# Optimization experiments

Hardware: AMD Instinct MI355X
Metric: run time of the kernel (lower is better)

Reference implementation:

```python
import jax, jax.numpy as jnp
import numpy as np


def setup_inputs() -> dict:
    key = jax.random.key(0)
    ks = jax.random.split(key, 6)
    B, Nab, Nag, d, K = 16, 16384, 16384, 128, 10
    return {
        "H1": jax.random.normal(ks[0], (B, Nab, d), jnp.float32),
        "H2": jax.random.normal(ks[1], (B, Nag, d), jnp.float32),
        "X1": jax.random.normal(ks[2], (B, Nab, 3), jnp.float32),
        "X2": jax.random.normal(ks[3], (B, Nag, 3), jnp.float32),
        "W1": jax.random.uniform(ks[4], (K, d, d), jnp.float32),
        "W2": jax.random.uniform(ks[5], (K, d, d), jnp.float32),
    }


def _kabsch(P, Q):
    # Rigid alignment: find R (3x3), t (3,) s.t. P @ R + t ~= Q (least squares).
    c1 = P.mean(axis=0)
    c2 = Q.mean(axis=0)
    Pc = P - c1
    Qc = Q - c2
    Hm = Pc.T @ Qc  # [3,3] covariance
    U, S, Vt = jnp.linalg.svd(Hm, full_matrices=False)
    sign = jnp.sign(jnp.linalg.det(U @ Vt))
    Dm = jnp.diag(jnp.concatenate([jnp.ones(2, dtype=P.dtype), sign[None]]))
    R = U @ Dm @ Vt
    t = c2 - c1 @ R
    return P @ R + t, R, t


def reference(H1, H2, X1, X2, W1, W2):
    # Keypoint cross-attention. Faithful to torch:
    #   alpha_1k = softmax( (H1 @ W1_k @ H2.T).mean(dim=1) / sqrt(d) )
    # Using mean-over-columns identity: (H1 @ W @ H2.T).mean(1) = H1 @ W @ mean(H2,0)
    d = H1.shape[-1]
    scale = 1.0 / np.sqrt(d)
    h2bar = H2.mean(axis=1)  # [B, d]
    h1bar = H1.mean(axis=1)  # [B, d]
    v1 = jnp.einsum('kde,be->bkd', W1, h2bar)          # W1_k @ mean(H2)
    s1 = jnp.einsum('bnd,bkd->bkn', H1, v1) * scale     # [B, K, Nab]
    a1 = jax.nn.softmax(s1, axis=-1)
    Y1 = jnp.einsum('bkn,bnc->bkc', a1, X1)             # [B, K, 3]
    v2 = jnp.einsum('kde,be->bkd', W2, h1bar)
    s2 = jnp.einsum('bmd,bkd->bkm', H2, v2) * scale     # [B, K, Nag]
    a2 = jax.nn.softmax(s2, axis=-1)
    Y2 = jnp.einsum('bkm,bmc->bkc', a2, X2)             # [B, K, 3]
    Y1_aligned, R, t = jax.vmap(_kabsch)(Y1, Y2)
    return jnp.stack([Y1, Y2, Y1_aligned], axis=1)      # [B, 3, K, 3]
```

## Files before the change

### kernel.cpp

```cpp
#include <hip/hip_runtime.h>
#include <math.h>

#define NB 16
#define NN 16384
#define DD 128
#define KK 10

#define WS_FLOATS 46336


__global__ __launch_bounds__(256) void k_mean2(const float* __restrict__ H2,
                                               float* __restrict__ hsum) {
    int tid = threadIdx.x, b = blockIdx.x;
    int batch = b >> 7, sub = b & 127;
    int c0 = tid & 15;
    int rofs = sub * 16 + (tid >> 4);
    const float4* H4 = (const float4*)H2 + (size_t)batch * (NN * (DD / 4));

    float4 a0 = make_float4(0.f, 0.f, 0.f, 0.f), a1 = a0;
    float4 h0 = H4[(size_t)rofs * 32 + c0];
    float4 h1 = H4[(size_t)rofs * 32 + c0 + 16];
#pragma unroll
    for (int s = 0; s < 8; ++s) {
        float4 g0, g1;
        if (s < 7) {
            int rn = (s + 1) * 2048 + rofs;
            g0 = H4[(size_t)rn * 32 + c0];
            g1 = H4[(size_t)rn * 32 + c0 + 16];
        } else {
            g0 = make_float4(0.f, 0.f, 0.f, 0.f); g1 = g0;
        }
        a0.x += h0.x; a0.y += h0.y; a0.z += h0.z; a0.w += h0.w;
        a1.x += h1.x; a1.y += h1.y; a1.z += h1.z; a1.w += h1.w;
        h0 = g0; h1 = g1;
    }
    a0.x += __shfl_xor(a0.x, 16); a0.x += __shfl_xor(a0.x, 32);
    a0.y += __shfl_xor(a0.y, 16); a0.y += __shfl_xor(a0.y, 32);
    a0.z += __shfl_xor(a0.z, 16); a0.z += __shfl_xor(a0.z, 32);
    a0.w += __shfl_xor(a0.w, 16); a0.w += __shfl_xor(a0.w, 32);
    a1.x += __shfl_xor(a1.x, 16); a1.x += __shfl_xor(a1.x, 32);
    a1.y += __shfl_xor(a1.y, 16); a1.y += __shfl_xor(a1.y, 32);
    a1.z += __shfl_xor(a1.z, 16); a1.z += __shfl_xor(a1.z, 32);
    a1.w += __shfl_xor(a1.w, 16); a1.w += __shfl_xor(a1.w, 32);

    __shared__ float4 cred[4][32];
    int wave = tid >> 6, lane = tid & 63;
    if (lane < 16) {
        cred[wave][lane] = a0;
        cred[wave][lane + 16] = a1;
    }
    __syncthreads();
    if (tid < 32) {
        float4 s0 = cred[0][tid], s1 = cred[1][tid], s2 = cred[2][tid], s3 = cred[3][tid];
        float* dst = hsum + (size_t)(NB + batch) * DD + tid * 4;
        atomicAdd(dst + 0, s0.x + s1.x + s2.x + s3.x);
        atomicAdd(dst + 1, s0.y + s1.y + s2.y + s3.y);
        atomicAdd(dst + 2, s0.z + s1.z + s2.z + s3.z);
        atomicAdd(dst + 3, s0.w + s1.w + s2.w + s3.w);
    }
}

__global__ __launch_bounds__(128) void k_v(const float* __restrict__ W1,
                                           const float* __restrict__ W2,
                                           const float* __restrict__ hsum,
                                           float* __restrict__ v, int p) {
    int bi = blockIdx.x;
    int b = bi / 10;
    int k = bi % 10;
    const float* W = (p ? W2 : W1) + (size_t)k * DD * DD;
    const float* hb = hsum + (size_t)((1 - p) * NB + b) * DD;
    __shared__ float4 h_s[32];
    int tid = threadIdx.x;
    if (tid < 32) h_s[tid] = ((const float4*)hb)[tid];
    __syncthreads();
    const float4* Wrow = (const float4*)(W + (size_t)tid * DD);
    float acc = 0.f;
#pragma unroll 8
    for (int e4 = 0; e4 < 32; ++e4) {
        float4 w4 = Wrow[e4];
        float4 h4 = h_s[e4];
        acc += w4.x * h4.x + w4.y * h4.y + w4.z * h4.z + w4.w * h4.w;
    }
    const float SCALE = (float)(1.0 / (16384.0 * 11.313708498984761));
    v[((size_t)(p * NB + b) * KK + k) * DD + tid] = acc * SCALE;
}

__global__ __launch_bounds__(256) void k_pass(const float* __restrict__ H,
                                              const float* __restrict__ X,
                                              const float* __restrict__ v,
                                              float* __restrict__ accg,
                                              float* __restrict__ hsumout,
                                              int do_sum) {
    int tid = threadIdx.x, b = blockIdx.x;
    int batch = b >> 7, sub = b & 127;
    int c0 = tid & 15;
    int rofs = sub * 16 + (tid >> 4);
    const float4* H4 = (const float4*)H + (size_t)batch * (NN * (DD / 4));
    const float* Xb = X + (size_t)batch * NN * 3;
    const float4* v4 = (const float4*)(v + (size_t)batch * KK * DD);

    float4 va[KK], vb[KK];
#pragma unroll
    for (int k = 0; k < KK; ++k) {
        va[k] = v4[k * 32 + c0];
        vb[k] = v4[k * 32 + c0 + 16];
    }

    float pSE[KK], pY0[KK], pY1[KK], pY2[KK];
#pragma unroll
    for (int k = 0; k < KK; ++k) { pSE[k] = 0.f; pY0[k] = 0.f; pY1[k] = 0.f; pY2[k] = 0.f; }
    float4 cs0 = make_float4(0.f, 0.f, 0.f, 0.f), cs1 = cs0;

    float4 h0 = H4[(size_t)rofs * 32 + c0];
    float4 h1 = H4[(size_t)rofs * 32 + c0 + 16];
    float x0 = Xb[rofs * 3 + 0], x1 = Xb[rofs * 3 + 1], x2 = Xb[rofs * 3 + 2];

#pragma unroll
    for (int s = 0; s < 8; ++s) {
        float4 g0, g1;
        float y0, y1, y2;
        if (s < 7) {
            int rn = (s + 1) * 2048 + rofs;
            g0 = H4[(size_t)rn * 32 + c0];
            g1 = H4[(size_t)rn * 32 + c0 + 16];
            y0 = Xb[rn * 3 + 0]; y1 = Xb[rn * 3 + 1]; y2 = Xb[rn * 3 + 2];
        } else {
            g0 = make_float4(0.f, 0.f, 0.f, 0.f); g1 = g0;
            y0 = 0.f; y1 = 0.f; y2 = 0.f;
        }
        float sc[KK];
#pragma unroll
        for (int k = 0; k < KK; ++k)
            sc[k] = h0.x * va[k].x + h0.y * va[k].y + h0.z * va[k].z + h0.w * va[k].w
                  + h1.x * vb[k].x + h1.y * vb[k].y + h1.z * vb[k].z + h1.w * vb[k].w;
#pragma unroll
        for (int k = 0; k < KK; ++k) {
            sc[k] += __shfl_xor(sc[k], 1);
            sc[k] += __shfl_xor(sc[k], 2);
            sc[k] += __shfl_xor(sc[k], 4);
            sc[k] += __shfl_xor(sc[k], 8);
        }
        if (c0 == 0) {
#pragma unroll
            for (int k = 0; k < KK; ++k) {
                float e = __expf(sc[k]);
                pSE[k] += e;
                pY0[k] += e * x0;
                pY1[k] += e * x1;
                pY2[k] += e * x2;
            }
        }
        if (do_sum) {
            cs0.x += h0.x; cs0.y += h0.y; cs0.z += h0.z; cs0.w += h0.w;
            cs1.x += h1.x; cs1.y += h1.y; cs1.z += h1.z; cs1.w += h1.w;
        }
        h0 = g0; h1 = g1; x0 = y0; x1 = y1; x2 = y2;
    }

#pragma unroll
    for (int k = 0; k < KK; ++k) {
        pSE[k] += __shfl_xor(pSE[k], 16); pSE[k] += __shfl_xor(pSE[k], 32);
        pY0[k] += __shfl_xor(pY0[k], 16); pY0[k] += __shfl_xor(pY0[k], 32);
        pY1[k] += __shfl_xor(pY1[k], 16); pY1[k] += __shfl_xor(pY1[k], 32);
        pY2[k] += __shfl_xor(pY2[k], 16); pY2[k] += __shfl_xor(pY2[k], 32);
    }
    __shared__ float red[4][40];
    __shared__ float4 cred[4][32];
    int wave = tid >> 6, lane = tid & 63;
    if (lane == 0) {
#pragma unroll
        for (int k = 0; k < KK; ++k) {
            red[wave][k] = pSE[k];
            red[wave][10 + k] = pY0[k];
            red[wave][20 + k] = pY1[k];
            red[wave][30 + k] = pY2[k];
        }
    }
    if (do_sum) {
        cs0.x += __shfl_xor(cs0.x, 16); cs0.x += __shfl_xor(cs0.x, 32);
        cs0.y += __shfl_xor(cs0.y, 16); cs0.y += __shfl_xor(cs0.y, 32);
        cs0.z += __shfl_xor(cs0.z, 16); cs0.z += __shfl_xor(cs0.z, 32);
        cs0.w += __shfl_xor(cs0.w, 16); cs0.w += __shfl_xor(cs0.w, 32);
        cs1.x += __shfl_xor(cs1.x, 16); cs1.x += __shfl_xor(cs1.x, 32);
        cs1.y += __shfl_xor(cs1.y, 16); cs1.y += __shfl_xor(cs1.y, 32);
        cs1.z += __shfl_xor(cs1.z, 16); cs1.z += __shfl_xor(cs1.z, 32);
        cs1.w += __shfl_xor(cs1.w, 16); cs1.w += __shfl_xor(cs1.w, 32);
        if (lane < 16) {
            cred[wave][lane] = cs0;
            cred[wave][lane + 16] = cs1;
        }
    }
    __syncthreads();
    if (tid < 40) {
        float ssum = red[0][tid] + red[1][tid] + red[2][tid] + red[3][tid];
        atomicAdd(accg + (size_t)batch * 40 + tid, ssum);
    }
    if (do_sum && tid >= 64 && tid < 96) {
        int c = tid - 64;
        float4 s0 = cred[0][c], s1 = cred[1][c], s2 = cred[2][c], s3 = cred[3][c];
        float* dst = hsumout + (size_t)batch * DD + c * 4;
        atomicAdd(dst + 0, s0.x + s1.x + s2.x + s3.x);
        atomicAdd(dst + 1, s0.y + s1.y + s2.y + s3.y);
        atomicAdd(dst + 2, s0.z + s1.z + s2.z + s3.z);
        atomicAdd(dst + 3, s0.w + s1.w + s2.w + s3.w);
    }
}

__global__ __launch_bounds__(64) void k_final(const float* __restrict__ accg,
                                              float* __restrict__ out) {
    int b = blockIdx.x;
    int tid = threadIdx.x;
    __shared__ float Ys[2][KK][3];
    if (tid < 2 * KK * 3) {
        int p = tid / 30;
        int r = tid % 30;
        int k = r / 3;
        int c = r % 3;
        const float* a = accg + (size_t)(p * NB + b) * 40;
        float val = a[10 + c * 10 + k] / a[k];
        Ys[p][k][c] = val;
        out[((size_t)(b * 3 + p) * KK + k) * 3 + c] = val;
    }
    __syncthreads();
    if (tid == 0) {
        double P[KK][3], Q[KK][3];
        double c1[3] = {0, 0, 0}, c2[3] = {0, 0, 0};
        for (int i = 0; i < KK; ++i)
            for (int c = 0; c < 3; ++c) {
                P[i][c] = (double)Ys[0][i][c];
                Q[i][c] = (double)Ys[1][i][c];
                c1[c] += P[i][c];
                c2[c] += Q[i][c];
            }
        for (int c = 0; c < 3; ++c) { c1[c] /= KK; c2[c] /= KK; }
        double A0[3][3];
        for (int a = 0; a < 3; ++a)
            for (int c = 0; c < 3; ++c) {
                double s = 0;
                for (int i = 0; i < KK; ++i) s += (P[i][a] - c1[a]) * (Q[i][c] - c2[c]);
                A0[a][c] = s;
            }
        double Bm[3][3], V[3][3];
        for (int a = 0; a < 3; ++a)
            for (int c = 0; c < 3; ++c) { Bm[a][c] = A0[a][c]; V[a][c] = (a == c) ? 1.0 : 0.0; }
        for (int sweep = 0; sweep < 16; ++sweep)
            for (int p = 0; p < 2; ++p)
                for (int q = p + 1; q < 3; ++q) {
                    double al = 0, be = 0, ga = 0;
                    for (int r = 0; r < 3; ++r) {
                        al += Bm[r][p] * Bm[r][p];
                        be += Bm[r][q] * Bm[r][q];
                        ga += Bm[r][p] * Bm[r][q];
                    }
                    if (fabs(ga) < 1e-300) continue;
                    double zeta = (be - al) / (2.0 * ga);
                    double t = copysign(1.0, zeta) / (fabs(zeta) + sqrt(1.0 + zeta * zeta));
                    double cs = 1.0 / sqrt(1.0 + t * t);
                    double sn = cs * t;
                    for (int r = 0; r < 3; ++r) {
                        double bp = Bm[r][p], bq = Bm[r][q];
                        Bm[r][p] = cs * bp - sn * bq;
                        Bm[r][q] = sn * bp + cs * bq;
                        double vp = V[r][p], vq = V[r][q];
                        V[r][p] = cs * vp - sn * vq;
                        V[r][q] = sn * vp + cs * vq;
                    }
                }
        double sig[3];
        for (int j = 0; j < 3; ++j) {
            sig[j] = sqrt(Bm[0][j] * Bm[0][j] + Bm[1][j] * Bm[1][j] + Bm[2][j] * Bm[2][j]);
            if (sig[j] < 1e-300) sig[j] = 1e-300;
        }
        int jmin = 0;
        if (sig[1] < sig[jmin]) jmin = 1;
        if (sig[2] < sig[jmin]) jmin = 2;
        double det = A0[0][0] * (A0[1][1] * A0[2][2] - A0[1][2] * A0[2][1])
                   - A0[0][1] * (A0[1][0] * A0[2][2] - A0[1][2] * A0[2][0])
                   + A0[0][2] * (A0[1][0] * A0[2][1] - A0[1][1] * A0[2][0]);
        double sgn = (det >= 0.0) ? 1.0 : -1.0;
        double R[3][3];
        for (int a = 0; a < 3; ++a)
            for (int c = 0; c < 3; ++c) {
                double s = 0;
                for (int j = 0; j < 3; ++j) {
                    double dj = (j == jmin) ? sgn : 1.0;
                    s += dj * (Bm[a][j] / sig[j]) * V[c][j];
                }
                R[a][c] = s;
            }
        for (int i = 0; i < KK; ++i)
            for (int c = 0; c < 3; ++c) {
                double s = c2[c];
                for (int a = 0; a < 3; ++a) s += (P[i][a] - c1[a]) * R[a][c];
                out[((size_t)(b * 3 + 2) * KK + i) * 3 + c] = (float)s;
            }
    }
}

extern "C" void kernel_launch(void* const* d_in, const int* in_sizes, int n_in,
                              void* d_out, int out_size, void* d_ws, size_t ws_size,
                              hipStream_t stream) {
    const float* H1 = (const float*)d_in[0];
    const float* H2 = (const float*)d_in[1];
    const float* X1 = (const float*)d_in[2];
    const float* X2 = (const float*)d_in[3];
    const float* W1 = (const float*)d_in[4];
    const float* W2 = (const float*)d_in[5];
    float* out = (float*)d_out;
    float* ws = (float*)d_ws;
    float* hsum = ws;
    float* v    = ws + 4096;
    float* accg = ws + 45056;

    hipMemsetAsync(d_ws, 0, WS_FLOATS * sizeof(float), stream);
    hipLaunchKernelGGL(k_mean2, dim3(2048), dim3(256), 0, stream, H2, hsum);
    hipLaunchKernelGGL(k_v, dim3(160), dim3(128), 0, stream, W1, W2, hsum, v, 0);
    hipLaunchKernelGGL(k_pass, dim3(2048), dim3(256), 0, stream,
                       H1, X1, v, accg, hsum, 1);
    hipLaunchKernelGGL(k_v, dim3(160), dim3(128), 0, stream, W1, W2, hsum, v, 1);
    hipLaunchKernelGGL(k_pass, dim3(2048), dim3(256), 0, stream,
                       H2, X2, v + (size_t)NB * KK * DD, accg + (size_t)NB * 40, hsum, 0);
    hipLaunchKernelGGL(k_final, dim3(16), dim3(64), 0, stream, accg, out);
}
```

Baseline: 400.6 us.

## Stream H tiles through LDS with async global_load_lds double buffering

The mean and pass kernels now load contiguous 32-row tiles of H into LDS using the global_load_lds builtin, double-buffered so the next tile is fetched while the current one is processed. Each block covers 256 contiguous rows instead of rows strided across the batch, which halves the grid to 1024 blocks. This targets memory-latency stalls in kernels that are bandwidth-bound. In exchange it adds 32KB of LDS per block and a barrier per tile, both of which can lower occupancy. The loads of X remain direct global reads.

```diff
diff --git a/kernel.cpp b/kernel.cpp
--- a/kernel.cpp
+++ b/kernel.cpp
@@ -8,46 +8,64 @@
 
 #define WS_FLOATS 46336
 
+#define TROWS 32
+#define TBYTES (TROWS * DD * 4)
+#define NTILES 8
+#define RPB 256
+
+typedef __attribute__((address_space(1))) const void* as1cv;
+typedef __attribute__((address_space(3))) void* as3v;
+
+__device__ __forceinline__ void stage_tile(const char* gtile, char* ltile,
+                                           int wave, int lane) {
+    const char* g = gtile + wave * 4096 + lane * 16;
+    char* l = ltile + wave * 4096;
+#pragma unroll
+    for (int i = 0; i < 4; ++i)
+        __builtin_amdgcn_global_load_lds((as1cv)(g + i * 1024),
+                                         (as3v)(l + i * 1024), 16, 0, 0);
+}
 
 __global__ __launch_bounds__(256) void k_mean2(const float* __restrict__ H2,
                                                float* __restrict__ hsum) {
-    int tid = threadIdx.x, b = blockIdx.x;
-    int batch = b >> 7, sub = b & 127;
+    __shared__ float buf[2][TROWS * DD];
+    __shared__ float4 cred[4][32];
+    int tid = threadIdx.x;
+    int wave = tid >> 6, lane = tid & 63;
+    int batch = blockIdx.x >> 6, sub = blockIdx.x & 63;
+    const char* Hbase = (const char*)(H2 + ((size_t)batch * NN + (size_t)sub * RPB) * DD);
+    int g = tid >> 4;
     int c0 = tid & 15;
-    int rofs = sub * 16 + (tid >> 4);
-    const float4* H4 = (const float4*)H2 + (size_t)batch * (NN * (DD / 4));
-
-    float4 a0 = make_float4(0.f, 0.f, 0.f, 0.f), a1 = a0;
-    float4 h0 = H4[(size_t)rofs * 32 + c0];
-    float4 h1 = H4[(size_t)rofs * 32 + c0 + 16];
-#pragma unroll
-    for (int s = 0; s < 8; ++s) {
-        float4 g0, g1;
-        if (s < 7) {
-            int rn = (s + 1) * 2048 + rofs;
-            g0 = H4[(size_t)rn * 32 + c0];
-            g1 = H4[(size_t)rn * 32 + c0 + 16];
-        } else {
-            g0 = make_float4(0.f, 0.f, 0.f, 0.f); g1 = g0;
-        }
-        a0.x += h0.x; a0.y += h0.y; a0.z += h0.z; a0.w += h0.w;
-        a1.x += h1.x; a1.y += h1.y; a1.z += h1.z; a1.w += h1.w;
-        h0 = g0; h1 = g1;
-    }
-    a0.x += __shfl_xor(a0.x, 16); a0.x += __shfl_xor(a0.x, 32);
-    a0.y += __shfl_xor(a0.y, 16); a0.y += __shfl_xor(a0.y, 32);
-    a0.z += __shfl_xor(a0.z, 16); a0.z += __shfl_xor(a0.z, 32);
-    a0.w += __shfl_xor(a0.w, 16); a0.w += __shfl_xor(a0.w, 32);
-    a1.x += __shfl_xor(a1.x, 16); a1.x += __shfl_xor(a1.x, 32);
-    a1.y += __shfl_xor(a1.y, 16); a1.y += __shfl_xor(a1.y, 32);
-    a1.z += __shfl_xor(a1.z, 16); a1.z += __shfl_xor(a1.z, 32);
-    a1.w += __shfl_xor(a1.w, 16); a1.w += __shfl_xor(a1.w, 32);
-
-    __shared__ float4 cred[4][32];
-    int wave = tid >> 6, lane = tid & 63;
+
+    float4 cs0 = make_float4(0.f, 0.f, 0.f, 0.f), cs1 = cs0;
+
+    stage_tile(Hbase, (char*)buf[0], wave, lane);
+    __syncthreads();
+    for (int t = 0; t < NTILES; ++t) {
+        if (t + 1 < NTILES)
+            stage_tile(Hbase + (size_t)(t + 1) * TBYTES, (char*)buf[(t + 1) & 1], wave, lane);
+        const float* B = buf[t & 1];
+#pragma unroll
+        for (int half = 0; half < 2; ++half) {
+            int r = g + half * 16;
+            float4 h0 = *(const float4*)(B + r * DD + c0 * 4);
+            float4 h1 = *(const float4*)(B + r * DD + 64 + c0 * 4);
+            cs0.x += h0.x; cs0.y += h0.y; cs0.z += h0.z; cs0.w += h0.w;
+            cs1.x += h1.x; cs1.y += h1.y; cs1.z += h1.z; cs1.w += h1.w;
+        }
+        __syncthreads();
+    }
+    cs0.x += __shfl_xor(cs0.x, 16); cs0.x += __shfl_xor(cs0.x, 32);
+    cs0.y += __shfl_xor(cs0.y, 16); cs0.y += __shfl_xor(cs0.y, 32);
+    cs0.z += __shfl_xor(cs0.z, 16); cs0.z += __shfl_xor(cs0.z, 32);
+    cs0.w += __shfl_xor(cs0.w, 16); cs0.w += __shfl_xor(cs0.w, 32);
+    cs1.x += __shfl_xor(cs1.x, 16); cs1.x += __shfl_xor(cs1.x, 32);
+    cs1.y += __shfl_xor(cs1.y, 16); cs1.y += __shfl_xor(cs1.y, 32);
+    cs1.z += __shfl_xor(cs1.z, 16); cs1.z += __shfl_xor(cs1.z, 32);
+    cs1.w += __shfl_xor(cs1.w, 16); cs1.w += __shfl_xor(cs1.w, 32);
     if (lane < 16) {
-        cred[wave][lane] = a0;
-        cred[wave][lane + 16] = a1;
+        cred[wave][lane] = cs0;
+        cred[wave][lane + 16] = cs1;
     }
     __syncthreads();
     if (tid < 32) {
@@ -91,13 +109,18 @@
                                               float* __restrict__ accg,
                                               float* __restrict__ hsumout,
                                               int do_sum) {
-    int tid = threadIdx.x, b = blockIdx.x;
-    int batch = b >> 7, sub = b & 127;
-    int c0 = tid & 15;
-    int rofs = sub * 16 + (tid >> 4);
-    const float4* H4 = (const float4*)H + (size_t)batch * (NN * (DD / 4));
+    __shared__ float buf[2][TROWS * DD];
+    __shared__ float red[4][40];
+    __shared__ float4 cred[4][32];
+    int tid = threadIdx.x;
+    int wave = tid >> 6, lane = tid & 63;
+    int batch = blockIdx.x >> 6, sub = blockIdx.x & 63;
+    int row0 = sub * RPB;
+    const char* Hbase = (const char*)(H + ((size_t)batch * NN + (size_t)row0) * DD);
     const float* Xb = X + (size_t)batch * NN * 3;
     const float4* v4 = (const float4*)(v + (size_t)batch * KK * DD);
+    int g = tid >> 4;
+    int c0 = tid & 15;
 
     float4 va[KK], vb[KK];
 #pragma unroll
@@ -111,50 +134,47 @@
     for (int k = 0; k < KK; ++k) { pSE[k] = 0.f; pY0[k] = 0.f; pY1[k] = 0.f; pY2[k] = 0.f; }
     float4 cs0 = make_float4(0.f, 0.f, 0.f, 0.f), cs1 = cs0;
 
-    float4 h0 = H4[(size_t)rofs * 32 + c0];
-    float4 h1 = H4[(size_t)rofs * 32 + c0 + 16];
-    float x0 = Xb[rofs * 3 + 0], x1 = Xb[rofs * 3 + 1], x2 = Xb[rofs * 3 + 2];
-
-#pragma unroll
-    for (int s = 0; s < 8; ++s) {
-        float4 g0, g1;
-        float y0, y1, y2;
-        if (s < 7) {
-            int rn = (s + 1) * 2048 + rofs;
-            g0 = H4[(size_t)rn * 32 + c0];
-            g1 = H4[(size_t)rn * 32 + c0 + 16];
-            y0 = Xb[rn * 3 + 0]; y1 = Xb[rn * 3 + 1]; y2 = Xb[rn * 3 + 2];
-        } else {
-            g0 = make_float4(0.f, 0.f, 0.f, 0.f); g1 = g0;
-            y0 = 0.f; y1 = 0.f; y2 = 0.f;
-        }
-        float sc[KK];
-#pragma unroll
-        for (int k = 0; k < KK; ++k)
-            sc[k] = h0.x * va[k].x + h0.y * va[k].y + h0.z * va[k].z + h0.w * va[k].w
-                  + h1.x * vb[k].x + h1.y * vb[k].y + h1.z * vb[k].z + h1.w * vb[k].w;
-#pragma unroll
-        for (int k = 0; k < KK; ++k) {
-            sc[k] += __shfl_xor(sc[k], 1);
-            sc[k] += __shfl_xor(sc[k], 2);
-            sc[k] += __shfl_xor(sc[k], 4);
-            sc[k] += __shfl_xor(sc[k], 8);
-        }
-        if (c0 == 0) {
+    stage_tile(Hbase, (char*)buf[0], wave, lane);
+    __syncthreads();
+    for (int t = 0; t < NTILES; ++t) {
+        if (t + 1 < NTILES)
+            stage_tile(Hbase + (size_t)(t + 1) * TBYTES, (char*)buf[(t + 1) & 1], wave, lane);
+        const float* B = buf[t & 1];
+#pragma unroll
+        for (int half = 0; half < 2; ++half) {
+            int r = g + half * 16;
+            float4 h0 = *(const float4*)(B + r * DD + c0 * 4);
+            float4 h1 = *(const float4*)(B + r * DD + 64 + c0 * 4);
+            int rowg = row0 + t * TROWS + r;
+            float x0 = Xb[rowg * 3 + 0], x1 = Xb[rowg * 3 + 1], x2 = Xb[rowg * 3 + 2];
+            float sc[KK];
+#pragma unroll
+            for (int k = 0; k < KK; ++k)
+                sc[k] = h0.x * va[k].x + h0.y * va[k].y + h0.z * va[k].z + h0.w * va[k].w
+                      + h1.x * vb[k].x + h1.y * vb[k].y + h1.z * vb[k].z + h1.w * vb[k].w;
 #pragma unroll
             for (int k = 0; k < KK; ++k) {
-                float e = __expf(sc[k]);
-                pSE[k] += e;
-                pY0[k] += e * x0;
-                pY1[k] += e * x1;
-                pY2[k] += e * x2;
-            }
-        }
-        if (do_sum) {
-            cs0.x += h0.x; cs0.y += h0.y; cs0.z += h0.z; cs0.w += h0.w;
-            cs1.x += h1.x; cs1.y += h1.y; cs1.z += h1.z; cs1.w += h1.w;
-        }
-        h0 = g0; h1 = g1; x0 = y0; x1 = y1; x2 = y2;
+                sc[k] += __shfl_xor(sc[k], 1);
+                sc[k] += __shfl_xor(sc[k], 2);
+                sc[k] += __shfl_xor(sc[k], 4);
+                sc[k] += __shfl_xor(sc[k], 8);
+            }
+            if (c0 == 0) {
+#pragma unroll
+                for (int k = 0; k < KK; ++k) {
+                    float e = __expf(sc[k]);
+                    pSE[k] += e;
+                    pY0[k] += e * x0;
+                    pY1[k] += e * x1;
+                    pY2[k] += e * x2;
+                }
+            }
+            if (do_sum) {
+                cs0.x += h0.x; cs0.y += h0.y; cs0.z += h0.z; cs0.w += h0.w;
+                cs1.x += h1.x; cs1.y += h1.y; cs1.z += h1.z; cs1.w += h1.w;
+            }
+        }
+        __syncthreads();
     }
 
 #pragma unroll
@@ -164,9 +184,6 @@
         pY1[k] += __shfl_xor(pY1[k], 16); pY1[k] += __shfl_xor(pY1[k], 32);
         pY2[k] += __shfl_xor(pY2[k], 16); pY2[k] += __shfl_xor(pY2[k], 32);
     }
-    __shared__ float red[4][40];
-    __shared__ float4 cred[4][32];
-    int wave = tid >> 6, lane = tid & 63;
     if (lane == 0) {
 #pragma unroll
         for (int k = 0; k < KK; ++k) {
@@ -313,12 +330,12 @@
     float* accg = ws + 45056;
 
     hipMemsetAsync(d_ws, 0, WS_FLOATS * sizeof(float), stream);
-    hipLaunchKernelGGL(k_mean2, dim3(2048), dim3(256), 0, stream, H2, hsum);
+    hipLaunchKernelGGL(k_mean2, dim3(1024), dim3(256), 0, stream, H2, hsum);
     hipLaunchKernelGGL(k_v, dim3(160), dim3(128), 0, stream, W1, W2, hsum, v, 0);
-    hipLaunchKernelGGL(k_pass, dim3(2048), dim3(256), 0, stream,
+    hipLaunchKernelGGL(k_pass, dim3(1024), dim3(256), 0, stream,
                        H1, X1, v, accg, hsum, 1);
     hipLaunchKernelGGL(k_v, dim3(160), dim3(128), 0, stream, W1, W2, hsum, v, 1);
-    hipLaunchKernelGGL(k_pass, dim3(2048), dim3(256), 0, stream,
+    hipLaunchKernelGGL(k_pass, dim3(1024), dim3(256), 0, stream,
                        H2, X2, v + (size_t)NB * KK * DD, accg + (size_t)NB * 40, hsum, 0);
     hipLaunchKernelGGL(k_final, dim3(16), dim3(64), 0, stream, accg, out);
 }
```

Result: slower. 409.6 us (+2.2%).
